# Kernel optimization log

Measured on AMD Instinct MI355X. Metric: run time of the kernel, lower is better.

The kernel has to match this reference:

```python
import jax, jax.numpy as jnp
import numpy as np

JITTER = 1e-5  # diagonal jitter added to Kzz for a stable solve


def _rbf(a, b, var, ls):
    # squared-exponential kernel: var * exp(-||a-b||^2 / (2 ls^2))
    sq = jnp.sum((a[:, None, :] - b[None, :, :]) ** 2, axis=-1)
    return var * jnp.exp(-0.5 * sq / (ls ** 2))


def setup_inputs() -> dict:
    key = jax.random.key(0)
    ks = jax.random.split(key, 6)
    n, q, p, m = 512, 8, 32, 64  # particles, state dim, obs dim, inducing pts
    pm = p * m
    x = jax.random.normal(ks[0], (n, q), jnp.float32)
    y = jax.random.normal(ks[1], (n, p), jnp.float32)
    z = jax.random.normal(ks[2], (n, pm, 1), jnp.float32)
    # posterior variance must be positive (it is divided by)
    gamma = jax.random.uniform(ks[3], (n, pm, 1), jnp.float32, 0.5, 1.5)
    inducing = jax.random.normal(ks[4], (m, q), jnp.float32)
    K = jnp.eye(p, dtype=jnp.float32)  # prior cross-dim covariance, K='I'
    var = jnp.float32(1.0)             # kernel variance
    lengthscale = jnp.float32(1.0)
    noise_var = jnp.float32(0.01)      # exp(logvar) = state/obs noise variance
    return dict(x=x, y=y, z=z, gamma=gamma, inducing=inducing, K=K,
                var=var, lengthscale=lengthscale, noise_var=noise_var)


def reference(x, y, z, gamma, inducing, K, var, lengthscale, noise_var):
    n = x.shape[0]
    m = inducing.shape[0]
    p = K.shape[0]
    Kfz = _rbf(x, inducing, var, lengthscale)                    # (n, m)
    Kzz = (_rbf(inducing, inducing, var, lengthscale)
           + JITTER * var * jnp.eye(m, dtype=x.dtype))           # (m, m)
    Kff_diag = var * jnp.ones((n,), x.dtype)                     # k(x,x)=var
    # A = (Kzz^{-1} Kfz^T)^T ; Kzz shared across the batch -> one solve
    A = jnp.linalg.solve(Kzz, Kfz.T).T                           # (n, m)
    B = Kff_diag - jnp.einsum('nm,nm->n', Kfz, A)                # (n,)
    # Kronecker expansion: kron(K, A[n,1,m]) -> (n, p, p*m)
    Abig = jnp.einsum('ij,nm->nijm', K, A).reshape(n, p, p * m)
    # diag of kron(K, B[n,1,1]) -> (n, p)
    b = B[:, None] * jnp.diagonal(K)[None, :]
    c = b + noise_var                                            # (n, p)
    # d = A^2 @ gamma + c
    d = jnp.einsum('npk,nk->np', Abig ** 2, gamma[..., 0]) + c   # (n, p)
    At = jnp.swapaxes(Abig, 1, 2)                                # (n, pm, p)
    GAT = gamma * At                                             # (n, pm, p)
    g = gamma - jnp.einsum('nkp,np->nk', GAT ** 2, 1.0 / d)[..., None]
    m_new = g * (z / gamma
                 + jnp.einsum('nkp,np->nk', At, y / c)[..., None])
    return (m_new, g)
```

## Files before the change

kernel.cpp:

```cpp
#include <hip/hip_runtime.h>

#define JITTER 1e-5f
#define NITER  10

__device__ __forceinline__ float fast_rcp(float v) {
#if __has_builtin(__builtin_amdgcn_rcpf)
    return __builtin_amdgcn_rcpf(v);
#else
    return 1.0f / v;
#endif
}

__global__ __launch_bounds__(256) void diag_sgp_cg1b(
    const float* __restrict__ x,
    const float* __restrict__ y,
    const float* __restrict__ z,
    const float* __restrict__ gamma,
    const float* __restrict__ inducing,
    const float* __restrict__ Kmat,
    const float* __restrict__ pvar,
    const float* __restrict__ pls,
    const float* __restrict__ pnoise,
    float* __restrict__ out,
    int n_total)
{
    const int tid = threadIdx.x;
    const int n   = blockIdx.x;

    const size_t base = (size_t)n * 2048 + tid * 8;
    const float4 g0 = *reinterpret_cast<const float4*>(gamma + base);
    const float4 g1 = *reinterpret_cast<const float4*>(gamma + base + 4);
    const float4 zv0 = *reinterpret_cast<const float4*>(z + base);
    const float4 zv1 = *reinterpret_cast<const float4*>(z + base + 4);

    __shared__ __align__(16) float Zl[64 * 8];
    __shared__ float Kl[32 * 33];
    __shared__ float xl[8], yl[32];
    __shared__ __align__(16) float a_sh[64];
    __shared__ __align__(16) float Mp_lds[2][64];
    __shared__ float t_sh[32], rc[32], rd[32], s1s[32], s2s[32];
    __shared__ float Bsh;

    for (int i = tid; i < 512; i += 256) Zl[i] = inducing[i];
    for (int i = tid; i < 1024; i += 256)
        Kl[(i >> 5) * 33 + (i & 31)] = Kmat[i];
    if (tid < 8)  xl[tid] = x[n * 8 + tid];
    if (tid < 32) yl[tid] = y[n * 32 + tid];
    const float var = pvar[0], ls = pls[0], nv = pnoise[0];
    const float sc = 0.5f / (ls * ls);
    __syncthreads();

    const int row = tid >> 2;
    const int q   = tid & 3;

    float zr[8];
    {
        const float4 za = *reinterpret_cast<const float4*>(&Zl[row * 8]);
        const float4 zb = *reinterpret_cast<const float4*>(&Zl[row * 8 + 4]);
        zr[0] = za.x; zr[1] = za.y; zr[2] = za.z; zr[3] = za.w;
        zr[4] = zb.x; zr[5] = zb.y; zr[6] = zb.z; zr[7] = zb.w;
    }

    float M_[16], e_t[16];
#pragma unroll
    for (int i = 0; i < 16; ++i) {
        const int c = q * 16 + i;
        const float4 r0 = *reinterpret_cast<const float4*>(&Zl[c * 8]);
        const float4 r1 = *reinterpret_cast<const float4*>(&Zl[c * 8 + 4]);
        float sm, se;
        {
            float d;
            d = zr[0] - r0.x; sm  = d * d;   d = xl[0] - r0.x; se  = d * d;
            d = zr[1] - r0.y; sm = fmaf(d, d, sm); d = xl[1] - r0.y; se = fmaf(d, d, se);
            d = zr[2] - r0.z; sm = fmaf(d, d, sm); d = xl[2] - r0.z; se = fmaf(d, d, se);
            d = zr[3] - r0.w; sm = fmaf(d, d, sm); d = xl[3] - r0.w; se = fmaf(d, d, se);
            d = zr[4] - r1.x; sm = fmaf(d, d, sm); d = xl[4] - r1.x; se = fmaf(d, d, se);
            d = zr[5] - r1.y; sm = fmaf(d, d, sm); d = xl[5] - r1.y; se = fmaf(d, d, se);
            d = zr[6] - r1.z; sm = fmaf(d, d, sm); d = xl[6] - r1.z; se = fmaf(d, d, se);
            d = zr[7] - r1.w; sm = fmaf(d, d, sm); d = xl[7] - r1.w; se = fmaf(d, d, se);
        }
        const float vm = __expf(-sm * sc);
        M_[i]  = (row == c) ? vm + JITTER : vm;
        e_t[i] = __expf(-se * sc);
    }

    float x_t[16], r_t[16], p_t[16];
    float rz;
    {
        float s = 0.f;
#pragma unroll
        for (int i = 0; i < 16; ++i) {
            x_t[i] = 0.f;
            r_t[i] = e_t[i];
            p_t[i] = e_t[i];
            s = fmaf(e_t[i], e_t[i], s);
        }
        s += __shfl_xor(s, 1);
        s += __shfl_xor(s, 2);
        rz = s;
    }

#pragma unroll
    for (int it = 0; it < NITER - 1; ++it) {
        const int buf = it & 1;
        {
            float mp = 0.f;
#pragma unroll
            for (int i = 0; i < 16; ++i) mp = fmaf(M_[i], p_t[i], mp);
            mp += __shfl_xor(mp, 1);
            mp += __shfl_xor(mp, 2);
            if (q == 0) Mp_lds[buf][row] = mp;
        }
        __syncthreads();

        const float4 ma = *reinterpret_cast<const float4*>(&Mp_lds[buf][q * 16 + 0]);
        const float4 mb = *reinterpret_cast<const float4*>(&Mp_lds[buf][q * 16 + 4]);
        const float4 mc = *reinterpret_cast<const float4*>(&Mp_lds[buf][q * 16 + 8]);
        const float4 md = *reinterpret_cast<const float4*>(&Mp_lds[buf][q * 16 + 12]);
        const float mpv[16] = {ma.x, ma.y, ma.z, ma.w, mb.x, mb.y, mb.z, mb.w,
                               mc.x, mc.y, mc.z, mc.w, md.x, md.y, md.z, md.w};

        float pap = 0.f;
#pragma unroll
        for (int i = 0; i < 16; ++i) pap = fmaf(p_t[i], mpv[i], pap);
        pap += __shfl_xor(pap, 1);
        pap += __shfl_xor(pap, 2);
        const float alpha = rz * fast_rcp(pap + 1e-30f);

        float rr = 0.f;
#pragma unroll
        for (int i = 0; i < 16; ++i) {
            x_t[i] = fmaf(alpha, p_t[i], x_t[i]);
            r_t[i] = fmaf(-alpha, mpv[i], r_t[i]);
            rr = fmaf(r_t[i], r_t[i], rr);
        }
        rr += __shfl_xor(rr, 1);
        rr += __shfl_xor(rr, 2);
        const float beta = rr * fast_rcp(rz + 1e-30f);
        rz = rr;
#pragma unroll
        for (int i = 0; i < 16; ++i) p_t[i] = fmaf(beta, p_t[i], r_t[i]);
    }

    {
        const int buf = (NITER - 1) & 1;
        float mp = 0.f;
#pragma unroll
        for (int i = 0; i < 16; ++i) mp = fmaf(M_[i], p_t[i], mp);
        mp += __shfl_xor(mp, 1);
        mp += __shfl_xor(mp, 2);
        if (q == 0) Mp_lds[buf][row] = mp;
        __syncthreads();

        const float4 ma = *reinterpret_cast<const float4*>(&Mp_lds[buf][q * 16 + 0]);
        const float4 mb = *reinterpret_cast<const float4*>(&Mp_lds[buf][q * 16 + 4]);
        const float4 mc = *reinterpret_cast<const float4*>(&Mp_lds[buf][q * 16 + 8]);
        const float4 md = *reinterpret_cast<const float4*>(&Mp_lds[buf][q * 16 + 12]);
        const float mpv[16] = {ma.x, ma.y, ma.z, ma.w, mb.x, mb.y, mb.z, mb.w,
                               mc.x, mc.y, mc.z, mc.w, md.x, md.y, md.z, md.w};
        float pap = 0.f;
#pragma unroll
        for (int i = 0; i < 16; ++i) pap = fmaf(p_t[i], mpv[i], pap);
        pap += __shfl_xor(pap, 1);
        pap += __shfl_xor(pap, 2);
        const float alpha = rz * fast_rcp(pap + 1e-30f);
#pragma unroll
        for (int i = 0; i < 16; ++i) x_t[i] = fmaf(alpha, p_t[i], x_t[i]);
    }

    {
        float s = 0.f;
#pragma unroll
        for (int i = 0; i < 16; ++i) s = fmaf(e_t[i], x_t[i], s);
        s += __shfl_xor(s, 1);
        s += __shfl_xor(s, 2);
        if (row == 0) {
#pragma unroll
            for (int i = 0; i < 16; ++i) a_sh[q * 16 + i] = x_t[i];
        }
        if (tid == 0) Bsh = var * (1.f - s);
    }
    __syncthreads();

    const int jrow = tid >> 3;
    float ga[8] = {g0.x, g0.y, g0.z, g0.w, g1.x, g1.y, g1.z, g1.w};
    const int ab = (tid & 7) * 8;
    const float4 a0 = *reinterpret_cast<const float4*>(&a_sh[ab]);
    const float4 a1 = *reinterpret_cast<const float4*>(&a_sh[ab + 4]);
    const float as[8] = {a0.x, a0.y, a0.z, a0.w, a1.x, a1.y, a1.z, a1.w};

    float pt = 0.f;
#pragma unroll
    for (int e = 0; e < 8; ++e) pt += as[e] * as[e] * ga[e];
    pt += __shfl_xor(pt, 1);
    pt += __shfl_xor(pt, 2);
    pt += __shfl_xor(pt, 4);
    if ((tid & 7) == 0) t_sh[jrow] = pt;
    __syncthreads();

    if (tid < 32) {
        float acc = 0.f;
        for (int jj = 0; jj < 32; ++jj) {
            const float kv = Kl[tid * 33 + jj];
            acc += kv * kv * t_sh[jj];
        }
        const float ci = Bsh * Kl[tid * 34] + nv;
        const float di = acc + ci;
        rc[tid] = yl[tid] / ci;
        rd[tid] = 1.0f / di;
    }
    __syncthreads();

    if (tid < 32) {
        float sa = 0.f, sb = 0.f;
        for (int i = 0; i < 32; ++i) {
            const float kv = Kl[i * 33 + tid];
            sa += kv * rc[i];
            sb += kv * kv * rd[i];
        }
        s1s[tid] = sa;
        s2s[tid] = sb;
    }
    __syncthreads();

    const float zv[8] = {zv0.x, zv0.y, zv0.z, zv0.w, zv1.x, zv1.y, zv1.z, zv1.w};
    const float s1j = s1s[jrow], s2j = s2s[jrow];
    float mn[8], gg[8];
#pragma unroll
    for (int e = 0; e < 8; ++e) {
        const float ge = ga[e];
        const float am = as[e];
        const float gm = ge * am;
        const float gv = ge - gm * gm * s2j;
        gg[e] = gv;
        mn[e] = gv * (zv[e] / ge + am * s1j);
    }

    float* o_m = out + base;
    float* o_g = out + (size_t)n_total * 2048 + base;
    *reinterpret_cast<float4*>(o_m)     = make_float4(mn[0], mn[1], mn[2], mn[3]);
    *reinterpret_cast<float4*>(o_m + 4) = make_float4(mn[4], mn[5], mn[6], mn[7]);
    *reinterpret_cast<float4*>(o_g)     = make_float4(gg[0], gg[1], gg[2], gg[3]);
    *reinterpret_cast<float4*>(o_g + 4) = make_float4(gg[4], gg[5], gg[6], gg[7]);
}

extern "C" void kernel_launch(void* const* d_in, const int* in_sizes, int n_in,
                              void* d_out, int out_size, void* d_ws, size_t ws_size,
                              hipStream_t stream)
{
    const float* x        = (const float*)d_in[0];
    const float* y        = (const float*)d_in[1];
    const float* z        = (const float*)d_in[2];
    const float* gamma    = (const float*)d_in[3];
    const float* inducing = (const float*)d_in[4];
    const float* Kmat     = (const float*)d_in[5];
    const float* pvar     = (const float*)d_in[6];
    const float* pls      = (const float*)d_in[7];
    const float* pnoise   = (const float*)d_in[8];
    float* out = (float*)d_out;

    const int n = in_sizes[0] / 8;
    diag_sgp_cg1b<<<dim3(n), dim3(256), 0, stream>>>(
        x, y, z, gamma, inducing, Kmat, pvar, pls, pnoise, out, n);
}
```

Before: 18.17 us.

## Split fused kernel into CG solve kernel and streaming epilogue kernel

```diff
diff --git a/kernel.cpp b/kernel.cpp
--- a/kernel.cpp
+++ b/kernel.cpp
@@ -2,6 +2,7 @@
 
 #define JITTER 1e-5f
 #define NITER  10
+#define WS_STRIDE 80
 
 __device__ __forceinline__ float fast_rcp(float v) {
 #if __has_builtin(__builtin_amdgcn_rcpf)
@@ -11,42 +12,22 @@
 #endif
 }
 
-__global__ __launch_bounds__(256) void diag_sgp_cg1b(
+__global__ __launch_bounds__(256) void diag_sgp_solve(
     const float* __restrict__ x,
-    const float* __restrict__ y,
-    const float* __restrict__ z,
-    const float* __restrict__ gamma,
     const float* __restrict__ inducing,
-    const float* __restrict__ Kmat,
     const float* __restrict__ pvar,
     const float* __restrict__ pls,
-    const float* __restrict__ pnoise,
-    float* __restrict__ out,
-    int n_total)
+    float* __restrict__ ws_a)
 {
     const int tid = threadIdx.x;
     const int n   = blockIdx.x;
 
-    const size_t base = (size_t)n * 2048 + tid * 8;
-    const float4 g0 = *reinterpret_cast<const float4*>(gamma + base);
-    const float4 g1 = *reinterpret_cast<const float4*>(gamma + base + 4);
-    const float4 zv0 = *reinterpret_cast<const float4*>(z + base);
-    const float4 zv1 = *reinterpret_cast<const float4*>(z + base + 4);
-
     __shared__ __align__(16) float Zl[64 * 8];
-    __shared__ float Kl[32 * 33];
-    __shared__ float xl[8], yl[32];
-    __shared__ __align__(16) float a_sh[64];
-    __shared__ __align__(16) float Mp_lds[2][64];
-    __shared__ float t_sh[32], rc[32], rd[32], s1s[32], s2s[32];
-    __shared__ float Bsh;
+    __shared__ float xl[8];
 
     for (int i = tid; i < 512; i += 256) Zl[i] = inducing[i];
-    for (int i = tid; i < 1024; i += 256)
-        Kl[(i >> 5) * 33 + (i & 31)] = Kmat[i];
-    if (tid < 8)  xl[tid] = x[n * 8 + tid];
-    if (tid < 32) yl[tid] = y[n * 32 + tid];
-    const float var = pvar[0], ls = pls[0], nv = pnoise[0];
+    if (tid < 8) xl[tid] = x[n * 8 + tid];
+    const float var = pvar[0], ls = pls[0];
     const float sc = 0.5f / (ls * ls);
     __syncthreads();
 
@@ -84,6 +65,7 @@
         e_t[i] = __expf(-se * sc);
     }
 
+    __shared__ __align__(16) float Mp_lds[2][64];
     float x_t[16], r_t[16], p_t[16];
     float rz;
     {
@@ -174,19 +156,53 @@
         for (int i = 0; i < 16; ++i) s = fmaf(e_t[i], x_t[i], s);
         s += __shfl_xor(s, 1);
         s += __shfl_xor(s, 2);
+        float* wp = ws_a + (size_t)n * WS_STRIDE;
         if (row == 0) {
 #pragma unroll
-            for (int i = 0; i < 16; ++i) a_sh[q * 16 + i] = x_t[i];
-        }
-        if (tid == 0) Bsh = var * (1.f - s);
-    }
-    __syncthreads();
+            for (int u = 0; u < 4; ++u)
+                *reinterpret_cast<float4*>(wp + q * 16 + u * 4) =
+                    make_float4(x_t[u * 4 + 0], x_t[u * 4 + 1],
+                                x_t[u * 4 + 2], x_t[u * 4 + 3]);
+        }
+        if (tid == 0) wp[64] = var * (1.f - s);
+    }
+}
+
+__global__ __launch_bounds__(256) void diag_sgp_epilogue(
+    const float* __restrict__ y,
+    const float* __restrict__ z,
+    const float* __restrict__ gamma,
+    const float* __restrict__ Kmat,
+    const float* __restrict__ pnoise,
+    const float* __restrict__ ws_a,
+    float* __restrict__ out,
+    int n_total)
+{
+    const int tid = threadIdx.x;
+    const int n   = blockIdx.x;
+
+    const size_t base = (size_t)n * 2048 + tid * 8;
+    const float4 g0 = *reinterpret_cast<const float4*>(gamma + base);
+    const float4 g1 = *reinterpret_cast<const float4*>(gamma + base + 4);
+    const float4 zv0 = *reinterpret_cast<const float4*>(z + base);
+    const float4 zv1 = *reinterpret_cast<const float4*>(z + base + 4);
+    const float* wp = ws_a + (size_t)n * WS_STRIDE;
+    const int ab = (tid & 7) * 8;
+    const float4 a0 = *reinterpret_cast<const float4*>(wp + ab);
+    const float4 a1 = *reinterpret_cast<const float4*>(wp + ab + 4);
+    const float Bv  = wp[64];
+    const float nv  = pnoise[0];
+
+    __shared__ float Kl[32 * 33];
+    __shared__ float yl[32];
+    __shared__ float t_sh[32], rc[32], rd[32], s1s[32], s2s[32];
+
+    for (int i = tid; i < 1024; i += 256)
+        Kl[(i >> 5) * 33 + (i & 31)] = Kmat[i];
+    if (tid < 32) yl[tid] = y[n * 32 + tid];
 
     const int jrow = tid >> 3;
     float ga[8] = {g0.x, g0.y, g0.z, g0.w, g1.x, g1.y, g1.z, g1.w};
-    const int ab = (tid & 7) * 8;
-    const float4 a0 = *reinterpret_cast<const float4*>(&a_sh[ab]);
-    const float4 a1 = *reinterpret_cast<const float4*>(&a_sh[ab + 4]);
     const float as[8] = {a0.x, a0.y, a0.z, a0.w, a1.x, a1.y, a1.z, a1.w};
 
     float pt = 0.f;
@@ -204,7 +220,7 @@
             const float kv = Kl[tid * 33 + jj];
             acc += kv * kv * t_sh[jj];
         }
-        const float ci = Bsh * Kl[tid * 34] + nv;
+        const float ci = Bv * Kl[tid * 34] + nv;
         const float di = acc + ci;
         rc[tid] = yl[tid] / ci;
         rd[tid] = 1.0f / di;
@@ -257,9 +273,12 @@
     const float* pvar     = (const float*)d_in[6];
     const float* pls      = (const float*)d_in[7];
     const float* pnoise   = (const float*)d_in[8];
-    float* out = (float*)d_out;
+    float* out  = (float*)d_out;
+    float* ws_a = (float*)d_ws;
 
     const int n = in_sizes[0] / 8;
-    diag_sgp_cg1b<<<dim3(n), dim3(256), 0, stream>>>(
-        x, y, z, gamma, inducing, Kmat, pvar, pls, pnoise, out, n);
-}
+
+    diag_sgp_solve<<<dim3(n), dim3(256), 0, stream>>>(x, inducing, pvar, pls, ws_a);
+    diag_sgp_epilogue<<<dim3(n), dim3(256), 0, stream>>>(
+        y, z, gamma, Kmat, pnoise, ws_a, out, n);
+}
```

Measured after the change: 19.88 us. 1.09x slower.

## Precompute Kzz inverse columns once, then apply via matvec per particle

Applied to the files above, without the earlier changes.

```diff
diff --git a/kernel.cpp b/kernel.cpp
--- a/kernel.cpp
+++ b/kernel.cpp
@@ -11,7 +11,150 @@
 #endif
 }
 
-__global__ __launch_bounds__(256) void diag_sgp_cg1b(
+__global__ __launch_bounds__(256) void minv_cols(
+    const float* __restrict__ inducing,
+    const float* __restrict__ pls,
+    float* __restrict__ minv)
+{
+    const int tid = threadIdx.x;
+    const int col = blockIdx.x;
+
+    __shared__ __align__(16) float Zl[64 * 8];
+    __shared__ __align__(16) float Mp_lds[2][64];
+
+    for (int i = tid; i < 512; i += 256) Zl[i] = inducing[i];
+    const float ls = pls[0];
+    const float sc = 0.5f / (ls * ls);
+    __syncthreads();
+
+    const int row = tid >> 2;
+    const int q   = tid & 3;
+
+    float zr[8];
+    {
+        const float4 za = *reinterpret_cast<const float4*>(&Zl[row * 8]);
+        const float4 zb = *reinterpret_cast<const float4*>(&Zl[row * 8 + 4]);
+        zr[0] = za.x; zr[1] = za.y; zr[2] = za.z; zr[3] = za.w;
+        zr[4] = zb.x; zr[5] = zb.y; zr[6] = zb.z; zr[7] = zb.w;
+    }
+
+    float M_[16];
+#pragma unroll
+    for (int i = 0; i < 16; ++i) {
+        const int c = q * 16 + i;
+        const float4 r0 = *reinterpret_cast<const float4*>(&Zl[c * 8]);
+        const float4 r1 = *reinterpret_cast<const float4*>(&Zl[c * 8 + 4]);
+        float sm;
+        {
+            float d;
+            d = zr[0] - r0.x; sm  = d * d;
+            d = zr[1] - r0.y; sm = fmaf(d, d, sm);
+            d = zr[2] - r0.z; sm = fmaf(d, d, sm);
+            d = zr[3] - r0.w; sm = fmaf(d, d, sm);
+            d = zr[4] - r1.x; sm = fmaf(d, d, sm);
+            d = zr[5] - r1.y; sm = fmaf(d, d, sm);
+            d = zr[6] - r1.z; sm = fmaf(d, d, sm);
+            d = zr[7] - r1.w; sm = fmaf(d, d, sm);
+        }
+        const float vm = __expf(-sm * sc);
+        M_[i] = (row == c) ? vm + JITTER : vm;
+    }
+
+    float x_t[16], r_t[16], p_t[16];
+    float rz;
+    {
+        float s = 0.f;
+#pragma unroll
+        for (int i = 0; i < 16; ++i) {
+            const float ev = (q * 16 + i == col) ? 1.f : 0.f;
+            x_t[i] = 0.f;
+            r_t[i] = ev;
+            p_t[i] = ev;
+            s = fmaf(ev, ev, s);
+        }
+        s += __shfl_xor(s, 1);
+        s += __shfl_xor(s, 2);
+        rz = s;
+    }
+
+#pragma unroll
+    for (int it = 0; it < NITER - 1; ++it) {
+        const int buf = it & 1;
+        {
+            float mp = 0.f;
+#pragma unroll
+            for (int i = 0; i < 16; ++i) mp = fmaf(M_[i], p_t[i], mp);
+            mp += __shfl_xor(mp, 1);
+            mp += __shfl_xor(mp, 2);
+            if (q == 0) Mp_lds[buf][row] = mp;
+        }
+        __syncthreads();
+
+        const float4 ma = *reinterpret_cast<const float4*>(&Mp_lds[buf][q * 16 + 0]);
+        const float4 mb = *reinterpret_cast<const float4*>(&Mp_lds[buf][q * 16 + 4]);
+        const float4 mc = *reinterpret_cast<const float4*>(&Mp_lds[buf][q * 16 + 8]);
+        const float4 md = *reinterpret_cast<const float4*>(&Mp_lds[buf][q * 16 + 12]);
+        const float mpv[16] = {ma.x, ma.y, ma.z, ma.w, mb.x, mb.y, mb.z, mb.w,
+                               mc.x, mc.y, mc.z, mc.w, md.x, md.y, md.z, md.w};
+
+        float pap = 0.f;
+#pragma unroll
+        for (int i = 0; i < 16; ++i) pap = fmaf(p_t[i], mpv[i], pap);
+        pap += __shfl_xor(pap, 1);
+        pap += __shfl_xor(pap, 2);
+        const float alpha = rz * fast_rcp(pap + 1e-30f);
+
+        float rr = 0.f;
+#pragma unroll
+        for (int i = 0; i < 16; ++i) {
+            x_t[i] = fmaf(alpha, p_t[i], x_t[i]);
+            r_t[i] = fmaf(-alpha, mpv[i], r_t[i]);
+            rr = fmaf(r_t[i], r_t[i], rr);
+        }
+        rr += __shfl_xor(rr, 1);
+        rr += __shfl_xor(rr, 2);
+        const float beta = rr * fast_rcp(rz + 1e-30f);
+        rz = rr;
+#pragma unroll
+        for (int i = 0; i < 16; ++i) p_t[i] = fmaf(beta, p_t[i], r_t[i]);
+    }
+    {
+        const int buf = (NITER - 1) & 1;
+        float mp = 0.f;
+#pragma unroll
+        for (int i = 0; i < 16; ++i) mp = fmaf(M_[i], p_t[i], mp);
+        mp += __shfl_xor(mp, 1);
+        mp += __shfl_xor(mp, 2);
+        if (q == 0) Mp_lds[buf][row] = mp;
+        __syncthreads();
+
+        const float4 ma = *reinterpret_cast<const float4*>(&Mp_lds[buf][q * 16 + 0]);
+        const float4 mb = *reinterpret_cast<const float4*>(&Mp_lds[buf][q * 16 + 4]);
+        const float4 mc = *reinterpret_cast<const float4*>(&Mp_lds[buf][q * 16 + 8]);
+        const float4 md = *reinterpret_cast<const float4*>(&Mp_lds[buf][q * 16 + 12]);
+        const float mpv[16] = {ma.x, ma.y, ma.z, ma.w, mb.x, mb.y, mb.z, mb.w,
+                               mc.x, mc.y, mc.z, mc.w, md.x, md.y, md.z, md.w};
+        float pap = 0.f;
+#pragma unroll
+        for (int i = 0; i < 16; ++i) pap = fmaf(p_t[i], mpv[i], pap);
+        pap += __shfl_xor(pap, 1);
+        pap += __shfl_xor(pap, 2);
+        const float alpha = rz * fast_rcp(pap + 1e-30f);
+#pragma unroll
+        for (int i = 0; i < 16; ++i) x_t[i] = fmaf(alpha, p_t[i], x_t[i]);
+    }
+
+    if (row == 0) {
+        float* wp = minv + (size_t)col * 64 + q * 16;
+#pragma unroll
+        for (int u = 0; u < 4; ++u)
+            *reinterpret_cast<float4*>(wp + u * 4) =
+                make_float4(x_t[u * 4 + 0], x_t[u * 4 + 1],
+                            x_t[u * 4 + 2], x_t[u * 4 + 3]);
+    }
+}
+
+__global__ __launch_bounds__(256) void diag_sgp_apply(
     const float* __restrict__ x,
     const float* __restrict__ y,
     const float* __restrict__ z,
@@ -21,25 +164,33 @@
     const float* __restrict__ pvar,
     const float* __restrict__ pls,
     const float* __restrict__ pnoise,
+    const float* __restrict__ minv,
     float* __restrict__ out,
     int n_total)
 {
     const int tid = threadIdx.x;
     const int n   = blockIdx.x;
+    const int row = tid >> 2;
+    const int q   = tid & 3;
 
     const size_t base = (size_t)n * 2048 + tid * 8;
     const float4 g0 = *reinterpret_cast<const float4*>(gamma + base);
     const float4 g1 = *reinterpret_cast<const float4*>(gamma + base + 4);
     const float4 zv0 = *reinterpret_cast<const float4*>(z + base);
     const float4 zv1 = *reinterpret_cast<const float4*>(z + base + 4);
+    const float* mvp = minv + (size_t)row * 64 + q * 16;
+    const float4 w0 = *reinterpret_cast<const float4*>(mvp);
+    const float4 w1 = *reinterpret_cast<const float4*>(mvp + 4);
+    const float4 w2 = *reinterpret_cast<const float4*>(mvp + 8);
+    const float4 w3 = *reinterpret_cast<const float4*>(mvp + 12);
+    const float W[16] = {w0.x, w0.y, w0.z, w0.w, w1.x, w1.y, w1.z, w1.w,
+                         w2.x, w2.y, w2.z, w2.w, w3.x, w3.y, w3.z, w3.w};
 
     __shared__ __align__(16) float Zl[64 * 8];
     __shared__ float Kl[32 * 33];
     __shared__ float xl[8], yl[32];
     __shared__ __align__(16) float a_sh[64];
-    __shared__ __align__(16) float Mp_lds[2][64];
     __shared__ float t_sh[32], rc[32], rd[32], s1s[32], s2s[32];
-    __shared__ float Bsh;
 
     for (int i = tid; i < 512; i += 256) Zl[i] = inducing[i];
     for (int i = tid; i < 1024; i += 256)
@@ -50,137 +201,52 @@
     const float sc = 0.5f / (ls * ls);
     __syncthreads();
 
-    const int row = tid >> 2;
-    const int q   = tid & 3;
-
-    float zr[8];
-    {
-        const float4 za = *reinterpret_cast<const float4*>(&Zl[row * 8]);
-        const float4 zb = *reinterpret_cast<const float4*>(&Zl[row * 8 + 4]);
-        zr[0] = za.x; zr[1] = za.y; zr[2] = za.z; zr[3] = za.w;
-        zr[4] = zb.x; zr[5] = zb.y; zr[6] = zb.z; zr[7] = zb.w;
-    }
-
-    float M_[16], e_t[16];
+    float e_t[16];
 #pragma unroll
     for (int i = 0; i < 16; ++i) {
         const int c = q * 16 + i;
         const float4 r0 = *reinterpret_cast<const float4*>(&Zl[c * 8]);
         const float4 r1 = *reinterpret_cast<const float4*>(&Zl[c * 8 + 4]);
-        float sm, se;
+        float se;
         {
             float d;
-            d = zr[0] - r0.x; sm  = d * d;   d = xl[0] - r0.x; se  = d * d;
-            d = zr[1] - r0.y; sm = fmaf(d, d, sm); d = xl[1] - r0.y; se = fmaf(d, d, se);
-            d = zr[2] - r0.z; sm = fmaf(d, d, sm); d = xl[2] - r0.z; se = fmaf(d, d, se);
-            d = zr[3] - r0.w; sm = fmaf(d, d, sm); d = xl[3] - r0.w; se = fmaf(d, d, se);
-            d = zr[4] - r1.x; sm = fmaf(d, d, sm); d = xl[4] - r1.x; se = fmaf(d, d, se);
-            d = zr[5] - r1.y; sm = fmaf(d, d, sm); d = xl[5] - r1.y; se = fmaf(d, d, se);
-            d = zr[6] - r1.z; sm = fmaf(d, d, sm); d = xl[6] - r1.z; se = fmaf(d, d, se);
-            d = zr[7] - r1.w; sm = fmaf(d, d, sm); d = xl[7] - r1.w; se = fmaf(d, d, se);
-        }
-        const float vm = __expf(-sm * sc);
-        M_[i]  = (row == c) ? vm + JITTER : vm;
+            d = xl[0] - r0.x; se  = d * d;
+            d = xl[1] - r0.y; se = fmaf(d, d, se);
+            d = xl[2] - r0.z; se = fmaf(d, d, se);
+            d = xl[3] - r0.w; se = fmaf(d, d, se);
+            d = xl[4] - r1.x; se = fmaf(d, d, se);
+            d = xl[5] - r1.y; se = fmaf(d, d, se);
+            d = xl[6] - r1.z; se = fmaf(d, d, se);
+            d = xl[7] - r1.w; se = fmaf(d, d, se);
+        }
         e_t[i] = __expf(-se * sc);
     }
 
-    float x_t[16], r_t[16], p_t[16];
-    float rz;
-    {
+    {
+        float ap = 0.f;
+#pragma unroll
+        for (int i = 0; i < 16; ++i) ap = fmaf(W[i], e_t[i], ap);
+        ap += __shfl_xor(ap, 1);
+        ap += __shfl_xor(ap, 2);
+        if (q == 0) a_sh[row] = ap;
+    }
+    __syncthreads();
+
+    float Bv;
+    {
+        const float4 aa = *reinterpret_cast<const float4*>(&a_sh[q * 16 + 0]);
+        const float4 ab4 = *reinterpret_cast<const float4*>(&a_sh[q * 16 + 4]);
+        const float4 ac = *reinterpret_cast<const float4*>(&a_sh[q * 16 + 8]);
+        const float4 ad = *reinterpret_cast<const float4*>(&a_sh[q * 16 + 12]);
+        const float av[16] = {aa.x, aa.y, aa.z, aa.w, ab4.x, ab4.y, ab4.z, ab4.w,
+                              ac.x, ac.y, ac.z, ac.w, ad.x, ad.y, ad.z, ad.w};
         float s = 0.f;
 #pragma unroll
-        for (int i = 0; i < 16; ++i) {
-            x_t[i] = 0.f;
-            r_t[i] = e_t[i];
-            p_t[i] = e_t[i];
-            s = fmaf(e_t[i], e_t[i], s);
-        }
+        for (int i = 0; i < 16; ++i) s = fmaf(e_t[i], av[i], s);
         s += __shfl_xor(s, 1);
         s += __shfl_xor(s, 2);
-        rz = s;
-    }
-
-#pragma unroll
-    for (int it = 0; it < NITER - 1; ++it) {
-        const int buf = it & 1;
-        {
-            float mp = 0.f;
-#pragma unroll
-            for (int i = 0; i < 16; ++i) mp = fmaf(M_[i], p_t[i], mp);
-            mp += __shfl_xor(mp, 1);
-            mp += __shfl_xor(mp, 2);
-            if (q == 0) Mp_lds[buf][row] = mp;
-        }
-        __syncthreads();
-
-        const float4 ma = *reinterpret_cast<const float4*>(&Mp_lds[buf][q * 16 + 0]);
-        const float4 mb = *reinterpret_cast<const float4*>(&Mp_lds[buf][q * 16 + 4]);
-        const float4 mc = *reinterpret_cast<const float4*>(&Mp_lds[buf][q * 16 + 8]);
-        const float4 md = *reinterpret_cast<const float4*>(&Mp_lds[buf][q * 16 + 12]);
-        const float mpv[16] = {ma.x, ma.y, ma.z, ma.w, mb.x, mb.y, mb.z, mb.w,
-                               mc.x, mc.y, mc.z, mc.w, md.x, md.y, md.z, md.w};
-
-        float pap = 0.f;
-#pragma unroll
-        for (int i = 0; i < 16; ++i) pap = fmaf(p_t[i], mpv[i], pap);
-        pap += __shfl_xor(pap, 1);
-        pap += __shfl_xor(pap, 2);
-        const float alpha = rz * fast_rcp(pap + 1e-30f);
-
-        float rr = 0.f;
-#pragma unroll
-        for (int i = 0; i < 16; ++i) {
-            x_t[i] = fmaf(alpha, p_t[i], x_t[i]);
-            r_t[i] = fmaf(-alpha, mpv[i], r_t[i]);
-            rr = fmaf(r_t[i], r_t[i], rr);
-        }
-        rr += __shfl_xor(rr, 1);
-        rr += __shfl_xor(rr, 2);
-        const float beta = rr * fast_rcp(rz + 1e-30f);
-        rz = rr;
-#pragma unroll
-        for (int i = 0; i < 16; ++i) p_t[i] = fmaf(beta, p_t[i], r_t[i]);
-    }
-
-    {
-        const int buf = (NITER - 1) & 1;
-        float mp = 0.f;
-#pragma unroll
-        for (int i = 0; i < 16; ++i) mp = fmaf(M_[i], p_t[i], mp);
-        mp += __shfl_xor(mp, 1);
-        mp += __shfl_xor(mp, 2);
-        if (q == 0) Mp_lds[buf][row] = mp;
-        __syncthreads();
-
-        const float4 ma = *reinterpret_cast<const float4*>(&Mp_lds[buf][q * 16 + 0]);
-        const float4 mb = *reinterpret_cast<const float4*>(&Mp_lds[buf][q * 16 + 4]);
-        const float4 mc = *reinterpret_cast<const float4*>(&Mp_lds[buf][q * 16 + 8]);
-        const float4 md = *reinterpret_cast<const float4*>(&Mp_lds[buf][q * 16 + 12]);
-        const float mpv[16] = {ma.x, ma.y, ma.z, ma.w, mb.x, mb.y, mb.z, mb.w,
-                               mc.x, mc.y, mc.z, mc.w, md.x, md.y, md.z, md.w};
-        float pap = 0.f;
-#pragma unroll
-        for (int i = 0; i < 16; ++i) pap = fmaf(p_t[i], mpv[i], pap);
-        pap += __shfl_xor(pap, 1);
-        pap += __shfl_xor(pap, 2);
-        const float alpha = rz * fast_rcp(pap + 1e-30f);
-#pragma unroll
-        for (int i = 0; i < 16; ++i) x_t[i] = fmaf(alpha, p_t[i], x_t[i]);
-    }
-
-    {
-        float s = 0.f;
-#pragma unroll
-        for (int i = 0; i < 16; ++i) s = fmaf(e_t[i], x_t[i], s);
-        s += __shfl_xor(s, 1);
-        s += __shfl_xor(s, 2);
-        if (row == 0) {
-#pragma unroll
-            for (int i = 0; i < 16; ++i) a_sh[q * 16 + i] = x_t[i];
-        }
-        if (tid == 0) Bsh = var * (1.f - s);
-    }
-    __syncthreads();
+        Bv = var * (1.f - s);
+    }
 
     const int jrow = tid >> 3;
     float ga[8] = {g0.x, g0.y, g0.z, g0.w, g1.x, g1.y, g1.z, g1.w};
@@ -204,7 +270,7 @@
             const float kv = Kl[tid * 33 + jj];
             acc += kv * kv * t_sh[jj];
         }
-        const float ci = Bsh * Kl[tid * 34] + nv;
+        const float ci = Bv * Kl[tid * 34] + nv;
         const float di = acc + ci;
         rc[tid] = yl[tid] / ci;
         rd[tid] = 1.0f / di;
@@ -257,9 +323,12 @@
     const float* pvar     = (const float*)d_in[6];
     const float* pls      = (const float*)d_in[7];
     const float* pnoise   = (const float*)d_in[8];
-    float* out = (float*)d_out;
+    float* out  = (float*)d_out;
+    float* minv = (float*)d_ws;
 
     const int n = in_sizes[0] / 8;
-    diag_sgp_cg1b<<<dim3(n), dim3(256), 0, stream>>>(
-        x, y, z, gamma, inducing, Kmat, pvar, pls, pnoise, out, n);
+
+    minv_cols<<<dim3(64), dim3(256), 0, stream>>>(inducing, pls, minv);
+    diag_sgp_apply<<<dim3(n), dim3(256), 0, stream>>>(
+        x, y, z, gamma, inducing, Kmat, pvar, pls, pnoise, minv, out, n);
 }
```

Result: slower. 20.95 us (+15.3%).
